# Performance work log

Hardware: AMD Instinct MI355X
Metric: run time of the kernel (lower is better)

## Reference

```python
import jax, jax.numpy as jnp
import numpy as np

H, N, CH = 256, 64, 1

def _r2c(x):
    return x[..., 0] + 1j * x[..., 1]

def setup_inputs() -> dict:
    key = jax.random.key(0)
    kA, kB, kC, kdt = jax.random.split(key, 4)
    # Build a Hurwitz A (skew-Hermitian - 0.5*I) so dA = (I-dt/2 A)^-1 (I+dt/2 A) has spectral radius < 1
    M = jax.random.normal(kA, (H, N, N, 2), dtype=jnp.float32) / np.float32(np.sqrt(N))
    Mc = _r2c(M)
    Ac = 0.5 * (Mc - jnp.conjugate(jnp.swapaxes(Mc, -1, -2))) - 0.5 * jnp.eye(N, dtype=Mc.dtype)
    A = jnp.stack([Ac.real, Ac.imag], axis=-1)  # (H,N,N,2)
    B = jax.random.normal(kB, (H, N, 2), dtype=jnp.float32)
    C = jax.random.normal(kC, (CH, H, N, 2), dtype=jnp.float32)
    # log_dt uniform in [log(1e-3), log(1e-1)], shape (H,1) per bilinear docstring
    log_dt = jax.random.uniform(kdt, (H, 1), dtype=jnp.float32,
                                minval=np.float32(np.log(1e-3)), maxval=np.float32(np.log(1e-1)))
    return {"A": A, "B": B, "C": C, "log_dt": log_dt, "L": 2048}

def _bilinear(dt, Ac, Bc):
    # dt: (H,1), Ac: (H,N,N) complex, Bc: (H,N) complex
    n = Ac.shape[-1]
    I = jnp.eye(n, dtype=Ac.dtype)
    half = (dt.astype(Ac.real.dtype) / 2)[:, None]  # (H,1,1)
    A_back = I - half * Ac
    A_fwd = I + half * Ac
    dB = dt.astype(Ac.dtype) * jnp.linalg.solve(A_back, Bc[..., None])[..., 0]  # (H,N)
    dA = jnp.linalg.solve(A_back, A_fwd)  # (H,N,N)
    return dA, dB

def _krylov(L, dA, dB):
    # x[..., l] = dA^l dB via squaring-doubling, matches S4 krylov math
    x = dB[..., None]  # (H,N,1)
    A_ = dA
    while x.shape[-1] < L:
        x = jnp.concatenate([x, jnp.einsum('hnm,hml->hnl', A_, x)], axis=-1)
        A_ = A_ @ A_
    return x[..., :L]

def reference(A, B, C, log_dt, L):
    Ac, Bc, Cc = _r2c(A), _r2c(B), _r2c(C)
    dt = jnp.exp(log_dt)  # (H,1)
    dA, dB = _bilinear(dt, Ac, Bc)
    x = _krylov(L, dA, dB)  # (H,N,L) complex
    # k[c,h,l] = sum_n C[c,h,n] * (dA^l dB)[h,n]; torch .float() on complex keeps real part
    k = jnp.einsum('chn,hnl->chl', Cc, x).real.astype(jnp.float32)
    return k
```

## Files before the change

kernel.cpp:

```cpp
#include <hip/hip_runtime.h>
#include <math.h>

#define NH   256
#define NN   64
#define LSEQ 2048
#define RS   72
#define RSW  68
#define PSZ  4608
#define NTH  1024

typedef __attribute__((ext_vector_type(8))) short short8;
typedef __attribute__((ext_vector_type(4))) float float4_t;
typedef __attribute__((ext_vector_type(16))) float float16_t;
typedef unsigned short u16;

#define MFMA(a,b,c)   __builtin_amdgcn_mfma_f32_16x16x32_bf16((a),(b),(c),0,0,0)
#define MFMA32(a,b,c) __builtin_amdgcn_mfma_f32_32x32x16_bf16((a),(b),(c),0,0,0)
#define PERM_HI 0x07060302u
#define PERM_LO 0x05040100u

static __device__ __forceinline__ void split2(float v, unsigned& hb, unsigned& lb) {
    hb = __float_as_uint(v) & 0xffff0000u;
    lb = __float_as_uint(v - __uint_as_float(hb));
}
static __device__ __forceinline__ unsigned pack2(float v) {
    unsigned hb, lb; split2(v, hb, lb);
    return __builtin_amdgcn_perm(hb, lb, PERM_HI);
}
static __device__ __forceinline__ float unpack2(unsigned w) {
    return __uint_as_float(w & 0xffff0000u) + __uint_as_float(w << 16);
}
static __device__ __forceinline__ short8 neg8(short8 v) {
    union { short8 s; int i[4]; } u; u.s = v;
#pragma unroll
    for (int m = 0; m < 4; ++m) u.i[m] ^= 0x80008000;
    return u.s;
}

static __device__ __forceinline__ void frag_packed(const unsigned* p, short8& hi, short8& lo) {
    const uint4* q = (const uint4*)p;
    uint4 d0 = q[0], d1 = q[1];
    unsigned e[8] = {d0.x, d0.y, d0.z, d0.w, d1.x, d1.y, d1.z, d1.w};
    union { short8 s; unsigned u[4]; } H, L;
#pragma unroll
    for (int m = 0; m < 4; ++m) {
        H.u[m] = __builtin_amdgcn_perm(e[2*m+1], e[2*m], PERM_HI);
        L.u[m] = __builtin_amdgcn_perm(e[2*m+1], e[2*m], PERM_LO);
    }
    hi = H.s; lo = L.s;
}

static __device__ __forceinline__ void frag_vals(const unsigned* e, short8& hi, short8& lo) {
    unsigned lb[8];
#pragma unroll
    for (int m = 0; m < 8; ++m) {
        unsigned hv = e[m] & 0xffff0000u;
        lb[m] = __float_as_uint(__uint_as_float(e[m]) - __uint_as_float(hv));
    }
    union { short8 s; unsigned u[4]; } H, L;
#pragma unroll
    for (int m = 0; m < 4; ++m) {
        H.u[m] = __builtin_amdgcn_perm(e[2*m+1],  e[2*m],  PERM_HI);
        L.u[m] = __builtin_amdgcn_perm(lb[2*m+1], lb[2*m], PERM_HI);
    }
    hi = H.s; lo = L.s;
}


template<bool IMAG>
static __device__ __forceinline__ void cmm_pp(
    const unsigned* __restrict__ Aprl, const unsigned* __restrict__ ApiI,
    const unsigned* __restrict__ Bprl, const unsigned* __restrict__ BpiI,
    int arow, int bcol, int fq,
    float4_t& accP, float4_t& accN, float4_t& accI1, float4_t& accI2)
{
#pragma unroll
    for (int ks = 0; ks < 2; ++ks) {
        const int k0 = ks*32 + fq*8;
        short8 Arh, Arl, Aih, Ail, Brh, Brl, Bih, Bil;
        frag_packed(Aprl + arow*RSW + k0, Arh, Arl);
        frag_packed(ApiI + arow*RSW + k0, Aih, Ail);
        frag_packed(Bprl + bcol*RSW + k0, Brh, Brl);
        frag_packed(BpiI + bcol*RSW + k0, Bih, Bil);
        accP = MFMA(Arh, Brh, accP); accP = MFMA(Arh, Brl, accP); accP = MFMA(Arl, Brh, accP);
        accN = MFMA(Aih, Bih, accN); accN = MFMA(Aih, Bil, accN); accN = MFMA(Ail, Bih, accN);
        if (IMAG) {
            accI1 = MFMA(Arh, Bih, accI1); accI1 = MFMA(Arh, Bil, accI1); accI1 = MFMA(Arl, Bih, accI1);
            accI2 = MFMA(Aih, Brh, accI2); accI2 = MFMA(Aih, Brl, accI2); accI2 = MFMA(Ail, Brh, accI2);
        }
    }
}

template<int BSZ, bool IMAG>
static __device__ __forceinline__ void cmm_ps(
    const unsigned* __restrict__ Aprl, const unsigned* __restrict__ ApiI,
    const u16* __restrict__ Bb,
    int arow, int bcol, int fq,
    float4_t& accP, float4_t& accN, float4_t& accI1, float4_t& accI2)
{
#pragma unroll
    for (int ks = 0; ks < 2; ++ks) {
        const int k0 = ks*32 + fq*8;
        short8 Arh, Arl, Aih, Ail;
        frag_packed(Aprl + arow*RSW + k0, Arh, Arl);
        frag_packed(ApiI + arow*RSW + k0, Aih, Ail);
        const u16* bp = Bb + bcol*RS + k0;
        short8 Brh = *(const short8*)(bp);
        short8 Brl = *(const short8*)(bp + BSZ);
        short8 Bih = *(const short8*)(bp + 2*BSZ);
        short8 Bil = *(const short8*)(bp + 3*BSZ);
        accP = MFMA(Arh, Brh, accP); accP = MFMA(Arh, Brl, accP); accP = MFMA(Arl, Brh, accP);
        accN = MFMA(Aih, Bih, accN); accN = MFMA(Aih, Bil, accN); accN = MFMA(Ail, Bih, accN);
        if (IMAG) {
            accI1 = MFMA(Arh, Bih, accI1); accI1 = MFMA(Arh, Bil, accI1); accI1 = MFMA(Arl, Bih, accI1);
            accI2 = MFMA(Aih, Brh, accI2); accI2 = MFMA(Aih, Brl, accI2); accI2 = MFMA(Ail, Brh, accI2);
        }
    }
}

static __device__ __forceinline__ void cmm_pair_pp(
    const unsigned* __restrict__ Aprl, const unsigned* __restrict__ ApiI,
    const unsigned* __restrict__ Bprl, const unsigned* __restrict__ BpiI,
    int arow, int bcol0, int fq,
    float4_t& P0, float4_t& N0, float4_t& I10, float4_t& I20,
    float4_t& P1, float4_t& N1, float4_t& I11, float4_t& I21)
{
#pragma unroll
    for (int ks = 0; ks < 2; ++ks) {
        const int k0 = ks*32 + fq*8;
        short8 Arh, Arl, Aih, Ail;
        frag_packed(Aprl + arow*RSW + k0, Arh, Arl);
        frag_packed(ApiI + arow*RSW + k0, Aih, Ail);
#pragma unroll
        for (int p = 0; p < 2; ++p) {
            short8 Brh, Brl, Bih, Bil;
            frag_packed(Bprl + (bcol0 + p*16)*RSW + k0, Brh, Brl);
            frag_packed(BpiI + (bcol0 + p*16)*RSW + k0, Bih, Bil);
            float4_t &aP = p ? P1 : P0, &aN = p ? N1 : N0;
            float4_t &aI1 = p ? I11 : I10, &aI2 = p ? I21 : I20;
            aP = MFMA(Arh, Brh, aP); aP = MFMA(Arh, Brl, aP); aP = MFMA(Arl, Brh, aP);
            aN = MFMA(Aih, Bih, aN); aN = MFMA(Aih, Bil, aN); aN = MFMA(Ail, Bih, aN);
            aI1 = MFMA(Arh, Bih, aI1); aI1 = MFMA(Arh, Bil, aI1); aI1 = MFMA(Arl, Bih, aI1);
            aI2 = MFMA(Aih, Brh, aI2); aI2 = MFMA(Aih, Brl, aI2); aI2 = MFMA(Ail, Brh, aI2);
        }
    }
}

template<int BSZ>
static __device__ __forceinline__ void cmm32_pk(
    const unsigned* __restrict__ Aprl, const unsigned* __restrict__ ApiI,
    const u16* __restrict__ Bb,
    int arow, int bcol, int khalf,
    float16_t& R, float16_t& I)
{
#pragma unroll
    for (int ks = 0; ks < 4; ++ks) {
        const int k0 = ks*16 + khalf;
        short8 Arh, Arl, Aih, Ail;
        frag_packed(Aprl + arow*RSW + k0, Arh, Arl);
        frag_packed(ApiI + arow*RSW + k0, Aih, Ail);
        const u16* bp = Bb + bcol*RS + k0;
        short8 Brh = *(const short8*)(bp);
        short8 Brl = *(const short8*)(bp + BSZ);
        short8 Bih = *(const short8*)(bp + 2*BSZ);
        short8 Bil = *(const short8*)(bp + 3*BSZ);
        short8 nAih = neg8(Aih), nAil = neg8(Ail);
        R = MFMA32(Arh, Brh, R);  I = MFMA32(Arh, Bih, I);
        R = MFMA32(Arh, Brl, R);  I = MFMA32(Arh, Bil, I);
        R = MFMA32(Arl, Brh, R);  I = MFMA32(Arl, Bih, I);
        R = MFMA32(nAih, Bih, R); I = MFMA32(Aih, Brh, I);
        R = MFMA32(nAih, Bil, R); I = MFMA32(Aih, Brl, I);
        R = MFMA32(nAil, Bih, R); I = MFMA32(Ail, Brh, I);
    }
}

static __device__ __forceinline__ void store_XT16(
    u16* XT, int rowbase, int bcol, const float* p_r, const float* p_i)
{
    unsigned hR[4], lR[4], hI[4], lI[4];
#pragma unroll
    for (int r = 0; r < 4; ++r) { split2(p_r[r], hR[r], lR[r]); split2(p_i[r], hI[r], lI[r]); }
    int tb = bcol*RS + rowbase;
    uint2 w;
    w.x = __builtin_amdgcn_perm(hR[1], hR[0], PERM_HI);
    w.y = __builtin_amdgcn_perm(hR[3], hR[2], PERM_HI);
    *(uint2*)&XT[tb] = w;
    w.x = __builtin_amdgcn_perm(lR[1], lR[0], PERM_HI);
    w.y = __builtin_amdgcn_perm(lR[3], lR[2], PERM_HI);
    *(uint2*)&XT[PSZ + tb] = w;
    w.x = __builtin_amdgcn_perm(hI[1], hI[0], PERM_HI);
    w.y = __builtin_amdgcn_perm(hI[3], hI[2], PERM_HI);
    *(uint2*)&XT[2*PSZ + tb] = w;
    w.x = __builtin_amdgcn_perm(lI[1], lI[0], PERM_HI);
    w.y = __builtin_amdgcn_perm(lI[3], lI[2], PERM_HI);
    *(uint2*)&XT[3*PSZ + tb] = w;
}

__global__ __launch_bounds__(NTH, 4) void ssm_kernel(
    const float* __restrict__ Ag,
    const float* __restrict__ Bg,
    const float* __restrict__ Cg,
    const float* __restrict__ LogDt,
    float* __restrict__ outp)
{
    __shared__ __align__(16) unsigned char lds[161792];
    unsigned* XRrl = (unsigned*)(lds);
    unsigned* XRiI = (unsigned*)(lds + 17408);
    u16*      XT0  = (u16*)(lds +  34816);
    u16*      XT1  = (u16*)(lds +  71680);
    unsigned* XFrl = (unsigned*)(lds + 108544);
    unsigned* XFiI = (unsigned*)(lds + 125952);
    unsigned* Gmrl = (unsigned*)(lds + 143360);
    unsigned* GmiI = (unsigned*)(lds + 152064);
    float* bvr = (float*)(lds + 160768);
    float* bvi = (float*)(lds + 161024);
    float* urr = (float*)(lds + 161280);
    float* uri = (float*)(lds + 161536);

    const int t    = threadIdx.x;
    const int lane = t & 63;
    const int wv   = t >> 6;
    const int fm   = lane & 15, fq = lane >> 4;
    const int h    = blockIdx.x;

    const int tip  = wv >> 1, tjp = wv & 1;
    const int parow = tip*16 + fm;
    const int pb0   = tjp*32 + fm;

    const int ti2 = (wv >> 1) & 1, tj2 = wv & 1;
    const int arow32 = ti2*32 + (lane & 31);
    const int bcol32 = tj2*32 + (lane & 31);
    const int khalf  = (lane >> 5) * 8;

    const float dt  = expf(LogDt[h]);
    const float hdt = 0.5f * dt;

    const float2* A2 = (const float2*)(Ag + (size_t)h * NN * NN * 2);
    const float4_t z4 = {0.f, 0.f, 0.f, 0.f};

#pragma unroll
    for (int e = 0; e < 4; ++e) {
        int idx = t + e*NTH;
        int i = idx >> 6, j = idx & 63;
        float2 a = A2[idx];
        float x1r = (i == j ? 1.0f : 0.0f) + hdt * a.x;
        float x1i = hdt * a.y;
        XRrl[i*RSW + j] = pack2(x1r);
        XRiI[i*RSW + j] = pack2(x1i);
        unsigned hb, lb;
        split2(x1r, hb, lb);
        XT0[j*RS + i]       = (u16)(hb >> 16);
        XT0[PSZ + j*RS + i] = (u16)(lb >> 16);
        split2(x1i, hb, lb);
        XT0[2*PSZ + j*RS + i] = (u16)(hb >> 16);
        XT0[3*PSZ + j*RS + i] = (u16)(lb >> 16);
    }
    if (t < NN) {
        float2 bv = ((const float2*)Bg)[h*NN + t];
        float2 cv = ((const float2*)Cg)[h*NN + t];
        bvr[t] = bv.x; bvi[t] = bv.y;
        Gmrl[t] = pack2(cv.x);
        GmiI[t] = pack2(cv.y);
    }
    __syncthreads();

    if (wv < 8) {
        float4_t P0 = z4, N0 = z4, I10 = z4, I20 = z4;
        float4_t P1 = z4, N1 = z4, I11 = z4, I21 = z4;
#pragma unroll
        for (int ks = 0; ks < 2; ++ks) {
            const int k0 = ks*32 + fq*8;
            unsigned vr[8], vi[8];
#pragma unroll
            for (int j = 0; j < 8; ++j) {
                float2 a = A2[parow*NN + k0 + j];
                vr[j] = __float_as_uint((parow == k0 + j ? 1.0f : 0.0f) - hdt * a.x);
                vi[j] = __float_as_uint(-hdt * a.y);
            }
            short8 Arh, Arl, Aih, Ail;
            frag_vals(vr, Arh, Arl);
            frag_vals(vi, Aih, Ail);
#pragma unroll
            for (int p = 0; p < 2; ++p) {
                const u16* bp = XT0 + (pb0 + p*16)*RS + k0;
                short8 Brh = *(const short8*)(bp);
                short8 Brl = *(const short8*)(bp + PSZ);
                short8 Bih = *(const short8*)(bp + 2*PSZ);
                short8 Bil = *(const short8*)(bp + 3*PSZ);
                float4_t &aP = p ? P1 : P0, &aN = p ? N1 : N0;
                float4_t &aI1 = p ? I11 : I10, &aI2 = p ? I21 : I20;
                aP = MFMA(Arh, Brh, aP); aP = MFMA(Arh, Brl, aP); aP = MFMA(Arl, Brh, aP);
                aN = MFMA(Aih, Bih, aN); aN = MFMA(Aih, Bil, aN); aN = MFMA(Ail, Bih, aN);
                aI1 = MFMA(Arh, Bih, aI1); aI1 = MFMA(Arh, Bil, aI1); aI1 = MFMA(Arl, Bih, aI1);
                aI2 = MFMA(Aih, Brh, aI2); aI2 = MFMA(Aih, Brl, aI2); aI2 = MFMA(Ail, Brh, aI2);
            }
        }
#pragma unroll
        for (int p = 0; p < 2; ++p) {
            const int bcol = pb0 + p*16;
            const float4_t &aP = p ? P1 : P0, &aN = p ? N1 : N0;
            const float4_t &aI1 = p ? I11 : I10, &aI2 = p ? I21 : I20;
#pragma unroll
            for (int rp = 0; rp < 2; ++rp) {
                int row0 = tip*16 + fq*4 + rp*2;
                uint2 w;
                w.x = pack2(aP[rp*2]   - aN[rp*2]);
                w.y = pack2(aP[rp*2+1] - aN[rp*2+1]);
                *(uint2*)&XFrl[bcol*RSW + row0] = w;
                w.x = pack2(aI1[rp*2]   + aI2[rp*2]);
                w.y = pack2(aI1[rp*2+1] + aI2[rp*2+1]);
                *(uint2*)&XFiI[bcol*RSW + row0] = w;
            }
        }
    }
    __syncthreads();

    {
        float4_t P0 = z4, N0 = z4, I10 = z4, I20 = z4;
        float4_t P1 = z4, N1 = z4, I11 = z4, I21 = z4;
        if (wv < 8)
            cmm_pair_pp(XRrl, XRiI, XFrl, XFiI, parow, pb0, fq, P0, N0, I10, I20, P1, N1, I11, I21);
        __syncthreads();
        if (wv < 8) {
#pragma unroll
            for (int p = 0; p < 2; ++p) {
                const int bcol = pb0 + p*16;
#pragma unroll
                for (int r = 0; r < 4; ++r) {
                    int row = tip*16 + fq*4 + r;
                    float vr = (p ? P1[r] : P0[r]) - (p ? N1[r] : N0[r]);
                    float vi = (p ? I11[r] : I10[r]) + (p ? I21[r] : I20[r]);
                    XRrl[row*RSW + bcol] = pack2(vr);
                    XRiI[row*RSW + bcol] = pack2(vi);
                }
            }
        }
    }
    __syncthreads();

    {
        float p_r[2][4], p_i[2][4];
        if (wv < 8) {
            float4_t P0 = z4, N0 = z4, I10 = z4, I20 = z4;
            float4_t P1 = z4, N1 = z4, I11 = z4, I21 = z4;
            cmm_pair_pp(XRrl, XRiI, XFrl, XFiI, parow, pb0, fq, P0, N0, I10, I20, P1, N1, I11, I21);
#pragma unroll
            for (int p = 0; p < 2; ++p) {
                const int bcol = pb0 + p*16;
                const float4_t &aP = p ? P1 : P0, &aN = p ? N1 : N0;
                const float4_t &aI1 = p ? I11 : I10, &aI2 = p ? I21 : I20;
#pragma unroll
                for (int r = 0; r < 4; ++r) {
                    int row = tip*16 + fq*4 + r;
                    float2 a = A2[row*NN + bcol];
                    float dd  = (row == bcol ? 1.0f : 0.0f);
                    float x1r = dd + hdt * a.x;
                    float x1i = hdt * a.y;
                    float vvr = unpack2(XRrl[row*RSW + bcol]);
                    float vvi = unpack2(XRiI[row*RSW + bcol]);
                    p_r[p][r] = 2.0f*(3.0f*x1r - 3.0f*vvr + (aP[r] - aN[r])) - dd;
                    p_i[p][r] = 2.0f*(3.0f*x1i - 3.0f*vvi + (aI1[r] + aI2[r]));
                }
                store_XT16(XT0, tip*16 + fq*4, bcol, p_r[p], p_i[p]);
            }
        }
        __syncthreads();
        if (wv < 8) {
#pragma unroll
            for (int p = 0; p < 2; ++p) {
                const int bcol = pb0 + p*16;
#pragma unroll
                for (int r = 0; r < 4; ++r) {
                    int row = tip*16 + fq*4 + r;
                    XRrl[row*RSW + bcol] = pack2(p_r[p][r]);
                    XRiI[row*RSW + bcol] = pack2(p_i[p][r]);
                }
            }
        }
    }
    __syncthreads();

    {
        int n = t >> 4, part = t & 15;
        uint4 Wr = *(const uint4*)(XRrl + n*RSW + part*4);
        uint4 Wi = *(const uint4*)(XRiI + n*RSW + part*4);
        unsigned wr[4] = {Wr.x, Wr.y, Wr.z, Wr.w};
        unsigned wi[4] = {Wi.x, Wi.y, Wi.z, Wi.w};
        float ar = 0.f, ai = 0.f;
#pragma unroll
        for (int e = 0; e < 4; ++e) {
            float mr = unpack2(wr[e]);
            float mi = unpack2(wi[e]);
            int k = part*4 + e;
            ar += mr*bvr[k] - mi*bvi[k];
            ai += mr*bvi[k] + mi*bvr[k];
        }
#pragma unroll
        for (int off = 8; off; off >>= 1) { ar += __shfl_xor(ar, off); ai += __shfl_xor(ai, off); }
        if (part == 0) { urr[n] = ar; uri[n] = ai; }
    }
    __syncthreads();

#pragma unroll 1
    for (int s = 1; s <= 9; ++s) {
        u16* XTcur = (s & 1) ? XT0 : XT1;
        u16* XTnx  = (s & 1) ? XT1 : XT0;
        float16_t sR, sI;
        if (wv >= 8) {
            if (s == 1) {
                int n = (t >> 3) & 63, part = t & 7;
                const unsigned* rp0 = XRrl + n*RSW + part*8;
                const unsigned* ip0 = XRiI + n*RSW + part*8;
                uint4 Wr0 = *(const uint4*)(rp0), Wr1 = *(const uint4*)(rp0 + 4);
                uint4 Wi0 = *(const uint4*)(ip0), Wi1 = *(const uint4*)(ip0 + 4);
                unsigned wr[8] = {Wr0.x, Wr0.y, Wr0.z, Wr0.w, Wr1.x, Wr1.y, Wr1.z, Wr1.w};
                unsigned wi[8] = {Wi0.x, Wi0.y, Wi0.z, Wi0.w, Wi1.x, Wi1.y, Wi1.z, Wi1.w};
                float ar = 0.f, ai = 0.f;
#pragma unroll
                for (int e = 0; e < 8; ++e) {
                    float mr = unpack2(wr[e]);
                    float mi = unpack2(wi[e]);
                    int k = part*8 + e;
                    ar += mr*urr[k] - mi*uri[k];
                    ai += mr*uri[k] + mi*urr[k];
                }
#pragma unroll
                for (int off = 4; off; off >>= 1) { ar += __shfl_xor(ar, off); ai += __shfl_xor(ai, off); }
                if (part == 0) {
                    float u_r = urr[n], u_i = uri[n];
                    XFrl[n]       = pack2(hdt*(u_r + bvr[n]));
                    XFiI[n]       = pack2(hdt*(u_i + bvi[n]));
                    XFrl[RSW + n] = pack2(hdt*(ar + u_r));
                    XFiI[RSW + n] = pack2(hdt*(ai + u_i));
                }
            } else if (s <= 6) {
                const int C = 1 << (s-1);
                const int w = wv - 8;
                const int nT = (s == 6) ? 8 : 4;
                if (w < nT) {
                    const int rt = w >> 2, ct = w & 3;
                    float4_t aP = z4, aN = z4, aI1 = z4, aI2 = z4;
                    cmm_pp<true>(XFrl, XFiI, XRrl, XRiI, rt*16 + fm, ct*16 + fm, fq, aP, aN, aI1, aI2);
#pragma unroll
                    for (int r = 0; r < 4; ++r) {
                        int orow = C + rt*16 + fq*4 + r;
                        int oc   = ct*16 + fm;
                        XFrl[orow*RSW + oc] = pack2(aP[r] - aN[r]);
                        XFiI[orow*RSW + oc] = pack2(aI1[r] + aI2[r]);
                    }
                }
            } else {
                const int C = 1 << (s-7);
                const int w = wv - 8;
                if (w < 4) {
                    float4_t aP = z4, aN = z4, aI1 = z4, aI2 = z4;
                    cmm_ps<PSZ, true>(Gmrl, GmiI, XTcur, fm, w*16 + fm, fq, aP, aN, aI1, aI2);
#pragma unroll
                    for (int r = 0; r < 4; ++r) {
                        int orow = C + fq*4 + r;
                        int oc   = w*16 + fm;
                        Gmrl[orow*RSW + oc] = pack2(aP[r] - aN[r]);
                        GmiI[orow*RSW + oc] = pack2(aI1[r] + aI2[r]);
                    }
                }
            }
        } else if (wv < 4) {
#pragma unroll
            for (int g = 0; g < 16; ++g) { sR[g] = 0.f; sI[g] = 0.f; }
            __builtin_amdgcn_s_setprio(1);
            cmm32_pk<PSZ>(XRrl, XRiI, XTcur, arow32, bcol32, khalf, sR, sI);
            __builtin_amdgcn_s_setprio(0);
            {
                const int col = tj2*32 + (lane & 31);
                const int hi4 = (lane >> 5) * 4;
#pragma unroll
                for (int q = 0; q < 4; ++q) {
                    float r4[4], i4[4];
#pragma unroll
                    for (int rr = 0; rr < 4; ++rr) { r4[rr] = sR[4*q+rr]; i4[rr] = sI[4*q+rr]; }
                    store_XT16(XTnx, ti2*32 + 8*q + hi4, col, r4, i4);
                }
            }
        }
        __syncthreads();
        if (wv < 4 && s < 9) {
            const int col = tj2*32 + (lane & 31);
            const int hi4 = (lane >> 5) * 4;
#pragma unroll
            for (int q = 0; q < 4; ++q) {
                const int rowb = ti2*32 + 8*q + hi4;
#pragma unroll
                for (int rr = 0; rr < 4; ++rr) {
                    XRrl[(rowb + rr)*RSW + col] = pack2(sR[4*q+rr]);
                    XRiI[(rowb + rr)*RSW + col] = pack2(sI[4*q+rr]);
                }
            }
        }
        __syncthreads();
    }

#pragma unroll 1
    for (int tt = 0; tt < 4; ++tt) {
        if (tt < 3 && wv < 4) {
            const int ab = tt * 8;
            float4_t aP = z4, aN = z4, aI1 = z4, aI2 = z4;
            cmm_ps<PSZ, true>(Gmrl, GmiI, XT1, ab + fm, wv*16 + fm, fq, aP, aN, aI1, aI2);
#pragma unroll
            for (int r = 0; r < 4; ++r) {
                int orow = 8 + ab + fq*4 + r;
                if (orow < 32) {
                    int oc = wv*16 + fm;
                    Gmrl[orow*RSW + oc] = pack2(aP[r] - aN[r]);
                    GmiI[orow*RSW + oc] = pack2(aI1[r] + aI2[r]);
                }
            }
        }
        if (wv >= 4 && wv < 8) {
            const int jb = tt * 8;
            int ga = jb + fm; if (ga > 31) ga = 31;
            float4_t aP = z4, aN = z4, aI1 = z4, aI2 = z4;
            __builtin_amdgcn_s_setprio(1);
            cmm_pp<false>(Gmrl, GmiI, XFrl, XFiI, ga, (wv-4)*16 + fm, fq, aP, aN, aI1, aI2);
            __builtin_amdgcn_s_setprio(0);
            if (fq < 2) {
                size_t base = (size_t)h * LSEQ;
#pragma unroll
                for (int r = 0; r < 4; ++r)
                    outp[base + (jb + fq*4 + r)*NN + (wv-4)*16 + fm] = aP[r] - aN[r];
            }
        }
        if (tt < 3) __syncthreads();
    }
}

extern "C" void kernel_launch(void* const* d_in, const int* in_sizes, int n_in,
                              void* d_out, int out_size, void* d_ws, size_t ws_size,
                              hipStream_t stream) {
    const float* A  = (const float*)d_in[0];
    const float* B  = (const float*)d_in[1];
    const float* C  = (const float*)d_in[2];
    const float* ld = (const float*)d_in[3];
    float* out = (float*)d_out;
    ssm_kernel<<<dim3(NH), dim3(NTH), 0, stream>>>(A, B, C, ld, out);
}
```

Measured before the change: 92.09 us.

## Store transposed X matrices in packed hi/lo u32 layout instead of split bf16 planes

After: 91.86 us. Within noise of the previous version (-0.3%).

```diff
diff --git a/kernel.cpp b/kernel.cpp
--- a/kernel.cpp
+++ b/kernel.cpp
@@ -4,9 +4,7 @@
 #define NH   256
 #define NN   64
 #define LSEQ 2048
-#define RS   72
 #define RSW  68
-#define PSZ  4608
 #define NTH  1024
 
 typedef __attribute__((ext_vector_type(8))) short short8;
@@ -91,33 +89,6 @@
     }
 }
 
-template<int BSZ, bool IMAG>
-static __device__ __forceinline__ void cmm_ps(
-    const unsigned* __restrict__ Aprl, const unsigned* __restrict__ ApiI,
-    const u16* __restrict__ Bb,
-    int arow, int bcol, int fq,
-    float4_t& accP, float4_t& accN, float4_t& accI1, float4_t& accI2)
-{
-#pragma unroll
-    for (int ks = 0; ks < 2; ++ks) {
-        const int k0 = ks*32 + fq*8;
-        short8 Arh, Arl, Aih, Ail;
-        frag_packed(Aprl + arow*RSW + k0, Arh, Arl);
-        frag_packed(ApiI + arow*RSW + k0, Aih, Ail);
-        const u16* bp = Bb + bcol*RS + k0;
-        short8 Brh = *(const short8*)(bp);
-        short8 Brl = *(const short8*)(bp + BSZ);
-        short8 Bih = *(const short8*)(bp + 2*BSZ);
-        short8 Bil = *(const short8*)(bp + 3*BSZ);
-        accP = MFMA(Arh, Brh, accP); accP = MFMA(Arh, Brl, accP); accP = MFMA(Arl, Brh, accP);
-        accN = MFMA(Aih, Bih, accN); accN = MFMA(Aih, Bil, accN); accN = MFMA(Ail, Bih, accN);
-        if (IMAG) {
-            accI1 = MFMA(Arh, Bih, accI1); accI1 = MFMA(Arh, Bil, accI1); accI1 = MFMA(Arl, Bih, accI1);
-            accI2 = MFMA(Aih, Brh, accI2); accI2 = MFMA(Aih, Brl, accI2); accI2 = MFMA(Ail, Brh, accI2);
-        }
-    }
-}
-
 static __device__ __forceinline__ void cmm_pair_pp(
     const unsigned* __restrict__ Aprl, const unsigned* __restrict__ ApiI,
     const unsigned* __restrict__ Bprl, const unsigned* __restrict__ BpiI,
@@ -146,54 +117,39 @@
     }
 }
 
-template<int BSZ>
-static __device__ __forceinline__ void cmm32_pk(
+static __device__ __forceinline__ void cmm32_pp(
     const unsigned* __restrict__ Aprl, const unsigned* __restrict__ ApiI,
-    const u16* __restrict__ Bb,
+    const unsigned* __restrict__ Bprl, const unsigned* __restrict__ BpiI,
     int arow, int bcol, int khalf,
     float16_t& R, float16_t& I)
 {
 #pragma unroll
     for (int ks = 0; ks < 4; ++ks) {
         const int k0 = ks*16 + khalf;
-        short8 Arh, Arl, Aih, Ail;
+        short8 Arh, Arl, Aih, Ail, Brh, Brl, Bih, Bil;
         frag_packed(Aprl + arow*RSW + k0, Arh, Arl);
         frag_packed(ApiI + arow*RSW + k0, Aih, Ail);
-        const u16* bp = Bb + bcol*RS + k0;
-        short8 Brh = *(const short8*)(bp);
-        short8 Brl = *(const short8*)(bp + BSZ);
-        short8 Bih = *(const short8*)(bp + 2*BSZ);
-        short8 Bil = *(const short8*)(bp + 3*BSZ);
+        frag_packed(Bprl + bcol*RSW + k0, Brh, Brl);
+        frag_packed(BpiI + bcol*RSW + k0, Bih, Bil);
         short8 nAih = neg8(Aih), nAil = neg8(Ail);
         R = MFMA32(Arh, Brh, R);  I = MFMA32(Arh, Bih, I);
         R = MFMA32(Arh, Brl, R);  I = MFMA32(Arh, Bil, I);
         R = MFMA32(Arl, Brh, R);  I = MFMA32(Arl, Bih, I);
         R = MFMA32(nAih, Bih, R); I = MFMA32(Aih, Brh, I);
-        R = MFMA32(nAih, Bil, R); I = MFMA32(Aih, Brl, I);
-        R = MFMA32(nAil, Bih, R); I = MFMA32(Ail, Brh, I);
-    }
-}
-
-static __device__ __forceinline__ void store_XT16(
-    u16* XT, int rowbase, int bcol, const float* p_r, const float* p_i)
+        R = MFMA32(nAih, Bil, R); I = MFMA32(Ail, Brh, I);
+        R = MFMA32(nAil, Bih, R); I = MFMA32(Aih, Brl, I);
+    }
+}
+
+static __device__ __forceinline__ void store_XTp(
+    unsigned* XTrl, unsigned* XTiI, int rowbase, int col,
+    const float* p_r, const float* p_i)
 {
-    unsigned hR[4], lR[4], hI[4], lI[4];
-#pragma unroll
-    for (int r = 0; r < 4; ++r) { split2(p_r[r], hR[r], lR[r]); split2(p_i[r], hI[r], lI[r]); }
-    int tb = bcol*RS + rowbase;
-    uint2 w;
-    w.x = __builtin_amdgcn_perm(hR[1], hR[0], PERM_HI);
-    w.y = __builtin_amdgcn_perm(hR[3], hR[2], PERM_HI);
-    *(uint2*)&XT[tb] = w;
-    w.x = __builtin_amdgcn_perm(lR[1], lR[0], PERM_HI);
-    w.y = __builtin_amdgcn_perm(lR[3], lR[2], PERM_HI);
-    *(uint2*)&XT[PSZ + tb] = w;
-    w.x = __builtin_amdgcn_perm(hI[1], hI[0], PERM_HI);
-    w.y = __builtin_amdgcn_perm(hI[3], hI[2], PERM_HI);
-    *(uint2*)&XT[2*PSZ + tb] = w;
-    w.x = __builtin_amdgcn_perm(lI[1], lI[0], PERM_HI);
-    w.y = __builtin_amdgcn_perm(lI[3], lI[2], PERM_HI);
-    *(uint2*)&XT[3*PSZ + tb] = w;
+    uint4 w;
+    w.x = pack2(p_r[0]); w.y = pack2(p_r[1]); w.z = pack2(p_r[2]); w.w = pack2(p_r[3]);
+    *(uint4*)&XTrl[col*RSW + rowbase] = w;
+    w.x = pack2(p_i[0]); w.y = pack2(p_i[1]); w.z = pack2(p_i[2]); w.w = pack2(p_i[3]);
+    *(uint4*)&XTiI[col*RSW + rowbase] = w;
 }
 
 __global__ __launch_bounds__(NTH, 4) void ssm_kernel(
@@ -203,19 +159,21 @@
     const float* __restrict__ LogDt,
     float* __restrict__ outp)
 {
-    __shared__ __align__(16) unsigned char lds[161792];
-    unsigned* XRrl = (unsigned*)(lds);
-    unsigned* XRiI = (unsigned*)(lds + 17408);
-    u16*      XT0  = (u16*)(lds +  34816);
-    u16*      XT1  = (u16*)(lds +  71680);
-    unsigned* XFrl = (unsigned*)(lds + 108544);
-    unsigned* XFiI = (unsigned*)(lds + 125952);
-    unsigned* Gmrl = (unsigned*)(lds + 143360);
-    unsigned* GmiI = (unsigned*)(lds + 152064);
-    float* bvr = (float*)(lds + 160768);
-    float* bvi = (float*)(lds + 161024);
-    float* urr = (float*)(lds + 161280);
-    float* uri = (float*)(lds + 161536);
+    __shared__ __align__(16) unsigned char lds[157696];
+    unsigned* XRrl  = (unsigned*)(lds);
+    unsigned* XRiI  = (unsigned*)(lds + 17408);
+    unsigned* XT0rl = (unsigned*)(lds + 34816);
+    unsigned* XT0iI = (unsigned*)(lds + 52224);
+    unsigned* XT1rl = (unsigned*)(lds + 69632);
+    unsigned* XT1iI = (unsigned*)(lds + 87040);
+    unsigned* XFrl  = (unsigned*)(lds + 104448);
+    unsigned* XFiI  = (unsigned*)(lds + 121856);
+    unsigned* Gmrl  = (unsigned*)(lds + 139264);
+    unsigned* GmiI  = (unsigned*)(lds + 147968);
+    float* bvr = (float*)(lds + 156672);
+    float* bvi = (float*)(lds + 156928);
+    float* urr = (float*)(lds + 157184);
+    float* uri = (float*)(lds + 157440);
 
     const int t    = threadIdx.x;
     const int lane = t & 63;
@@ -245,15 +203,11 @@
         float2 a = A2[idx];
         float x1r = (i == j ? 1.0f : 0.0f) + hdt * a.x;
         float x1i = hdt * a.y;
-        XRrl[i*RSW + j] = pack2(x1r);
-        XRiI[i*RSW + j] = pack2(x1i);
-        unsigned hb, lb;
-        split2(x1r, hb, lb);
-        XT0[j*RS + i]       = (u16)(hb >> 16);
-        XT0[PSZ + j*RS + i] = (u16)(lb >> 16);
-        split2(x1i, hb, lb);
-        XT0[2*PSZ + j*RS + i] = (u16)(hb >> 16);
-        XT0[3*PSZ + j*RS + i] = (u16)(lb >> 16);
+        unsigned wr = pack2(x1r), wi = pack2(x1i);
+        XRrl[i*RSW + j] = wr;
+        XRiI[i*RSW + j] = wi;
+        XT0rl[j*RSW + i] = wr;
+        XT0iI[j*RSW + i] = wi;
     }
     if (t < NN) {
         float2 bv = ((const float2*)Bg)[h*NN + t];
@@ -282,11 +236,9 @@
             frag_vals(vi, Aih, Ail);
 #pragma unroll
             for (int p = 0; p < 2; ++p) {
-                const u16* bp = XT0 + (pb0 + p*16)*RS + k0;
-                short8 Brh = *(const short8*)(bp);
-                short8 Brl = *(const short8*)(bp + PSZ);
-                short8 Bih = *(const short8*)(bp + 2*PSZ);
-                short8 Bil = *(const short8*)(bp + 3*PSZ);
+                short8 Brh, Brl, Bih, Bil;
+                frag_packed(XT0rl + (pb0 + p*16)*RSW + k0, Brh, Brl);
+                frag_packed(XT0iI + (pb0 + p*16)*RSW + k0, Bih, Bil);
                 float4_t &aP = p ? P1 : P0, &aN = p ? N1 : N0;
                 float4_t &aI1 = p ? I11 : I10, &aI2 = p ? I21 : I20;
                 aP = MFMA(Arh, Brh, aP); aP = MFMA(Arh, Brl, aP); aP = MFMA(Arl, Brh, aP);
@@ -361,7 +313,7 @@
                     p_r[p][r] = 2.0f*(3.0f*x1r - 3.0f*vvr + (aP[r] - aN[r])) - dd;
                     p_i[p][r] = 2.0f*(3.0f*x1i - 3.0f*vvi + (aI1[r] + aI2[r]));
                 }
-                store_XT16(XT0, tip*16 + fq*4, bcol, p_r[p], p_i[p]);
+                store_XTp(XT0rl, XT0iI, tip*16 + fq*4, bcol, p_r[p], p_i[p]);
             }
         }
         __syncthreads();
@@ -403,8 +355,10 @@
 
 #pragma unroll 1
     for (int s = 1; s <= 9; ++s) {
-        u16* XTcur = (s & 1) ? XT0 : XT1;
-        u16* XTnx  = (s & 1) ? XT1 : XT0;
+        unsigned* XTcrl = (s & 1) ? XT0rl : XT1rl;
+        unsigned* XTciI = (s & 1) ? XT0iI : XT1iI;
+        unsigned* XTnrl = (s & 1) ? XT1rl : XT0rl;
+        unsigned* XTniI = (s & 1) ? XT1iI : XT0iI;
         float16_t sR, sI;
         if (wv >= 8) {
             if (s == 1) {
@@ -454,7 +408,7 @@
                 const int w = wv - 8;
                 if (w < 4) {
                     float4_t aP = z4, aN = z4, aI1 = z4, aI2 = z4;
-                    cmm_ps<PSZ, true>(Gmrl, GmiI, XTcur, fm, w*16 + fm, fq, aP, aN, aI1, aI2);
+                    cmm_pp<true>(Gmrl, GmiI, XTcrl, XTciI, fm, w*16 + fm, fq, aP, aN, aI1, aI2);
 #pragma unroll
                     for (int r = 0; r < 4; ++r) {
                         int orow = C + fq*4 + r;
@@ -468,7 +422,7 @@
 #pragma unroll
             for (int g = 0; g < 16; ++g) { sR[g] = 0.f; sI[g] = 0.f; }
             __builtin_amdgcn_s_setprio(1);
-            cmm32_pk<PSZ>(XRrl, XRiI, XTcur, arow32, bcol32, khalf, sR, sI);
+            cmm32_pp(XRrl, XRiI, XTcrl, XTciI, arow32, bcol32, khalf, sR, sI);
             __builtin_amdgcn_s_setprio(0);
             {
                 const int col = tj2*32 + (lane & 31);
@@ -478,7 +432,7 @@
                     float r4[4], i4[4];
 #pragma unroll
                     for (int rr = 0; rr < 4; ++rr) { r4[rr] = sR[4*q+rr]; i4[rr] = sI[4*q+rr]; }
-                    store_XT16(XTnx, ti2*32 + 8*q + hi4, col, r4, i4);
+                    store_XTp(XTnrl, XTniI, ti2*32 + 8*q + hi4, col, r4, i4);
                 }
             }
         }
@@ -504,7 +458,7 @@
         if (tt < 3 && wv < 4) {
             const int ab = tt * 8;
             float4_t aP = z4, aN = z4, aI1 = z4, aI2 = z4;
-            cmm_ps<PSZ, true>(Gmrl, GmiI, XT1, ab + fm, wv*16 + fm, fq, aP, aN, aI1, aI2);
+            cmm_pp<true>(Gmrl, GmiI, XT1rl, XT1iI, ab + fm, wv*16 + fm, fq, aP, aN, aI1, aI2);
 #pragma unroll
             for (int r = 0; r < 4; ++r) {
                 int orow = 8 + ab + fq*4 + r;
```
